# Optimization experiments

Hardware: AMD Instinct MI355X
Metric: run time of the kernel (lower is better)

The kernel has to match this reference:

```python
import jax, jax.numpy as jnp
import numpy as np

N_NODES = 50000


def gcn_conv(h, src, dst, W, b, n):
    # PyG GCNConv: x' = D^{-1/2} (A + I) D^{-1/2} (h W) + b
    x = h @ W  # [N, out]
    deg = jax.ops.segment_sum(jnp.ones_like(src, dtype=x.dtype), dst, num_segments=n) + 1.0  # self-loop
    dis = deg ** -0.5
    norm = dis[src] * dis[dst]  # [E]
    msg = x[src] * norm[:, None]  # [E, out]
    agg = jax.ops.segment_sum(msg, dst, num_segments=n)
    agg = agg + x * (dis * dis)[:, None]  # self-loop term: 1/deg_i * x_i
    return agg + b


def setup_inputs() -> dict:
    key = jax.random.key(0)
    ks = jax.random.split(key, 8)
    n, e = N_NODES, 800000
    d_in, d_rni, h = 128, 32, 256
    x = jax.random.normal(ks[0], (n, d_in), dtype=jnp.float32)
    rni = jax.random.normal(ks[1], (n, d_rni), dtype=jnp.float32)
    edge_index = jax.random.randint(ks[2], (2, e), 0, n, dtype=jnp.int64)
    s1 = (d_in + d_rni) ** -0.5
    s2 = h ** -0.5
    W1 = jax.random.normal(ks[3], (d_in + d_rni, h), dtype=jnp.float32) * s1
    b1 = jnp.zeros((h,), dtype=jnp.float32)
    W2 = jax.random.normal(ks[4], (h, h), dtype=jnp.float32) * s2
    b2 = jnp.zeros((h,), dtype=jnp.float32)
    W_out = jax.random.normal(ks[5], (h, h), dtype=jnp.float32) * s2
    b_out = jnp.zeros((h,), dtype=jnp.float32)
    return {"x": x, "rni": rni, "edge_index": edge_index, "W1": W1, "b1": b1,
            "W2": W2, "b2": b2, "W_out": W_out, "b_out": b_out}


def reference(x, rni, edge_index, W1, b1, W2, b2, W_out, b_out):
    n = x.shape[0]
    src, dst = edge_index[0], edge_index[1]
    h = jnp.concatenate([x, rni], axis=-1)  # RNI concat
    h = jax.nn.relu(gcn_conv(h, src, dst, W1, b1, n))
    h = jax.nn.relu(gcn_conv(h, src, dst, W2, b2, n))
    return h @ W_out + b_out
```

## Files before the change

kernel.cpp:

```cpp
#include <hip/hip_runtime.h>
#include <hip/hip_bf16.h>
#include <hip/hip_fp16.h>
#include <math.h>

#define D_IN   128
#define D_RNI  32
#define HID    256

typedef _Float16 half8 __attribute__((ext_vector_type(8)));
typedef float    f32x4 __attribute__((ext_vector_type(4)));

__global__ void k_prep(const unsigned int* __restrict__ ew, int nwords, int* __restrict__ mode,
                       const float* __restrict__ W1, __half* __restrict__ W1t,
                       const float* __restrict__ W2, __half* __restrict__ W2t,
                       const float* __restrict__ Wo, __half* __restrict__ Wot) {
    int b = blockIdx.x;
    if (b == 0) {
        __shared__ unsigned int red[256];
        unsigned int acc = 0;
        for (int i = threadIdx.x; i < 1024; i += 256) {
            int idx = 2 * i + 1;
            if (idx < nwords) acc |= ew[idx];
        }
        red[threadIdx.x] = acc;
        __syncthreads();
        for (int s = 128; s > 0; s >>= 1) {
            if (threadIdx.x < s) red[threadIdx.x] |= red[threadIdx.x + s];
            __syncthreads();
        }
        if (threadIdx.x == 0) *mode = (red[0] == 0u) ? 1 : 0;
        return;
    }
    int i = (b - 1) * 256 + threadIdx.x;
    const int T1 = (D_IN + D_RNI) * HID;
    const int T2 = HID * HID;
    if (i < T1) {
        int k = i / HID, nn = i - k * HID;
        W1t[(size_t)nn * (D_IN + D_RNI) + k] = __float2half(W1[i]);
    } else if (i < T1 + T2) {
        int j = i - T1;
        int k = j / HID, nn = j - k * HID;
        W2t[(size_t)nn * HID + k] = __float2half(W2[j]);
    } else {
        int j = i - T1 - T2;
        int k = j / HID, nn = j - k * HID;
        Wot[(size_t)nn * HID + k] = __float2half(Wo[j]);
    }
}

__global__ void k_count(const unsigned int* __restrict__ ew, const int* __restrict__ mode_p,
                        int* __restrict__ counts, int e) {
    int mode = *mode_p;
    int i = blockIdx.x * 256 + threadIdx.x;
    if (i >= e) return;
    int d = mode ? (int)ew[2 * ((size_t)e + i)] : (int)ew[(size_t)e + i];
    atomicAdd(&counts[d], 1);
}

__global__ __launch_bounds__(1024) void k_scan1(const int* __restrict__ counts,
                                                int* __restrict__ incl,
                                                int* __restrict__ bsum, int n) {
    __shared__ int sd[1024];
    int t = threadIdx.x;
    int i = blockIdx.x * 1024 + t;
    int v = (i < n) ? counts[i] : 0;
    sd[t] = v;
    __syncthreads();
    for (int off = 1; off < 1024; off <<= 1) {
        int tmp = (t >= off) ? sd[t - off] : 0;
        __syncthreads();
        sd[t] += tmp;
        __syncthreads();
    }
    if (i < n) incl[i] = sd[t];
    if (t == 1023) bsum[blockIdx.x] = sd[1023];
}

__global__ void k_scan3(const int* __restrict__ counts, const int* __restrict__ incl,
                        const int* __restrict__ bsum,
                        int* __restrict__ rowptr, int* __restrict__ cursor,
                        float* __restrict__ dis, int n, int nb) {
    __shared__ int pre_s, tot_s;
    int t = threadIdx.x;
    int c = (blockIdx.x * 256) >> 10;
    if (t < 64) {
        int v   = (t < nb) ? bsum[t] : 0;
        int pre = (t < c)  ? v : 0;
        int tot = v;
        #pragma unroll
        for (int m = 32; m > 0; m >>= 1) {
            pre += __shfl_down(pre, m);
            tot += __shfl_down(tot, m);
        }
        if (t == 0) { pre_s = pre; tot_s = tot; }
    }
    __syncthreads();
    int i = blockIdx.x * 256 + t;
    if (i >= n) return;
    int excl = incl[i] - counts[i] + pre_s;
    rowptr[i] = excl;
    cursor[i] = excl;
    dis[i] = 1.0f / sqrtf((float)(counts[i] + 1));
    if (i == 0) rowptr[n] = tot_s;
}

__global__ void k_scatter(const unsigned int* __restrict__ ew, const int* __restrict__ mode_p,
                          int* __restrict__ cursor, int* __restrict__ csr, int e) {
    int mode = *mode_p;
    int i = blockIdx.x * 256 + threadIdx.x;
    if (i >= e) return;
    int s, d;
    if (mode) {
        s = (int)ew[2 * (size_t)i];
        d = (int)ew[2 * ((size_t)e + i)];
    } else {
        s = (int)ew[(size_t)i];
        d = (int)ew[(size_t)e + i];
    }
    int pos = atomicAdd(&cursor[d], 1);
    csr[pos] = s;
}

#define KT 32
#define LSTR 40
template <bool A_F32, bool ADD_BIAS, bool HALF_OUT>
__global__ __launch_bounds__(512, 4) void k_mgemm(const void* __restrict__ Av, int strideA, int KA,
                                                  const void* __restrict__ A2v, int strideA2,
                                                  const __half* __restrict__ Bt,
                                                  const float* __restrict__ bias,
                                                  void* Cv, int M, int K) {
    __shared__ __half As[2][128 * LSTR];
    __shared__ __half Bs[2][256 * LSTR];
    int tid = threadIdx.x;
    int wave = tid >> 6, lane = tid & 63;
    int wm = wave >> 2, wn = wave & 3;
    int q = lane >> 4, m16 = lane & 15;
    int r0 = blockIdx.x * 128;

    int ar  = tid >> 2, akq = (tid & 3) * 8;
    int br  = tid >> 1, bkq = (tid & 1) * 16;

    int arow = r0 + ar; if (arow >= M) arow = M - 1;

    f32x4 acc[4][4] = {};

    float4 afr0, afr1;
    uint4  areg;
    uint4  breg0, breg1;

    auto loadA = [&](int k0) {
        if (A_F32) {
            const float* src; int stride, kk0;
            if (k0 < KA) { src = (const float*)Av;  stride = strideA;  kk0 = k0; }
            else         { src = (const float*)A2v; stride = strideA2; kk0 = k0 - KA; }
            const float* p = &src[(size_t)arow * stride + kk0 + akq];
            afr0 = *reinterpret_cast<const float4*>(p);
            afr1 = *reinterpret_cast<const float4*>(p + 4);
        } else {
            const __half* src = (const __half*)Av;
            areg = *reinterpret_cast<const uint4*>(&src[(size_t)arow * strideA + k0 + akq]);
        }
    };
    auto loadB = [&](int k0) {
        const __half* p = &Bt[(size_t)br * K + k0 + bkq];
        breg0 = *reinterpret_cast<const uint4*>(p);
        breg1 = *reinterpret_cast<const uint4*>(p + 8);
    };
    auto writeLDS = [&](int buf) {
        if (A_F32) {
            union { __half2 h2[4]; uint4 u; } uu;
            uu.h2[0] = __floats2half2_rn(afr0.x, afr0.y);
            uu.h2[1] = __floats2half2_rn(afr0.z, afr0.w);
            uu.h2[2] = __floats2half2_rn(afr1.x, afr1.y);
            uu.h2[3] = __floats2half2_rn(afr1.z, afr1.w);
            *reinterpret_cast<uint4*>(&As[buf][ar * LSTR + akq]) = uu.u;
        } else {
            *reinterpret_cast<uint4*>(&As[buf][ar * LSTR + akq]) = areg;
        }
        *reinterpret_cast<uint4*>(&Bs[buf][br * LSTR + bkq])     = breg0;
        *reinterpret_cast<uint4*>(&Bs[buf][br * LSTR + bkq + 8]) = breg1;
    };

    const int S = K / KT;
    loadA(0); loadB(0);
    writeLDS(0);
    __syncthreads();

    for (int t = 0; t < S; ++t) {
        int cur = t & 1;
        if (t + 1 < S) { loadA((t + 1) * KT); loadB((t + 1) * KT); }

        half8 af[4], bf[4];
        #pragma unroll
        for (int mi = 0; mi < 4; ++mi)
            af[mi] = *reinterpret_cast<const half8*>(&As[cur][(wm * 64 + mi * 16 + m16) * LSTR + q * 8]);
        #pragma unroll
        for (int ni = 0; ni < 4; ++ni)
            bf[ni] = *reinterpret_cast<const half8*>(&Bs[cur][(wn * 64 + ni * 16 + m16) * LSTR + q * 8]);
        #pragma unroll
        for (int mi = 0; mi < 4; ++mi)
            #pragma unroll
            for (int ni = 0; ni < 4; ++ni)
                acc[mi][ni] = __builtin_amdgcn_mfma_f32_16x16x32_f16(af[mi], bf[ni], acc[mi][ni], 0, 0, 0);

        if (t + 1 < S) writeLDS(cur ^ 1);
        __syncthreads();
    }

    #pragma unroll
    for (int mi = 0; mi < 4; ++mi) {
        #pragma unroll
        for (int r = 0; r < 4; ++r) {
            int row = r0 + wm * 64 + mi * 16 + q * 4 + r;
            if (row >= M) continue;
            #pragma unroll
            for (int ni = 0; ni < 4; ++ni) {
                int col = wn * 64 + ni * 16 + m16;
                float v = acc[mi][ni][r];
                if (ADD_BIAS) v += bias[col];
                if (HALF_OUT) ((__half*)Cv)[(size_t)row * HID + col] = __float2half(v);
                else          ((float*)Cv)[(size_t)row * HID + col] = v;
            }
        }
    }
}

__global__ __launch_bounds__(256) void k_agg(const __half* __restrict__ xh,
                                             const int* __restrict__ rowptr,
                                             const int* __restrict__ csr,
                                             const float* __restrict__ dis,
                                             const float* __restrict__ bias,
                                             __half* __restrict__ outh, int n) {
    int i = blockIdx.x * 4 + (threadIdx.x >> 6);
    if (i >= n) return;
    int lane = threadIdx.x & 63;
    int c4 = lane * 4;
    float disd = dis[i];
    int e0 = rowptr[i], e1 = rowptr[i + 1];

    float acc0, acc1, acc2, acc3;
    {
        uint2 v = *reinterpret_cast<const uint2*>(&xh[(size_t)i * HID + c4]);
        float2 f0 = __half22float2(*reinterpret_cast<__half2*>(&v.x));
        float2 f1 = __half22float2(*reinterpret_cast<__half2*>(&v.y));
        float ws = disd * disd;
        acc0 = f0.x * ws; acc1 = f0.y * ws; acc2 = f1.x * ws; acc3 = f1.y * ws;
    }

    for (int e = e0; e < e1; e += 64) {
        int cnt = min(64, e1 - e);
        int sreg = 0; float wreg = 0.0f;
        if (lane < cnt) {
            sreg = csr[e + lane];
            wreg = dis[sreg] * disd;
        }
        int j = 0;
        for (; j + 4 <= cnt; j += 4) {
            int   s0 = __shfl(sreg, j + 0), s1 = __shfl(sreg, j + 1);
            int   s2 = __shfl(sreg, j + 2), s3 = __shfl(sreg, j + 3);
            float w0 = __shfl(wreg, j + 0), w1 = __shfl(wreg, j + 1);
            float w2 = __shfl(wreg, j + 2), w3 = __shfl(wreg, j + 3);
            uint2 v0 = *reinterpret_cast<const uint2*>(&xh[(size_t)s0 * HID + c4]);
            uint2 v1 = *reinterpret_cast<const uint2*>(&xh[(size_t)s1 * HID + c4]);
            uint2 v2 = *reinterpret_cast<const uint2*>(&xh[(size_t)s2 * HID + c4]);
            uint2 v3 = *reinterpret_cast<const uint2*>(&xh[(size_t)s3 * HID + c4]);
            float2 a0 = __half22float2(*reinterpret_cast<__half2*>(&v0.x));
            float2 b0 = __half22float2(*reinterpret_cast<__half2*>(&v0.y));
            float2 a1 = __half22float2(*reinterpret_cast<__half2*>(&v1.x));
            float2 b1 = __half22float2(*reinterpret_cast<__half2*>(&v1.y));
            float2 a2 = __half22float2(*reinterpret_cast<__half2*>(&v2.x));
            float2 b2 = __half22float2(*reinterpret_cast<__half2*>(&v2.y));
            float2 a3 = __half22float2(*reinterpret_cast<__half2*>(&v3.x));
            float2 b3 = __half22float2(*reinterpret_cast<__half2*>(&v3.y));
            acc0 = fmaf(a0.x, w0, acc0); acc1 = fmaf(a0.y, w0, acc1);
            acc2 = fmaf(b0.x, w0, acc2); acc3 = fmaf(b0.y, w0, acc3);
            acc0 = fmaf(a1.x, w1, acc0); acc1 = fmaf(a1.y, w1, acc1);
            acc2 = fmaf(b1.x, w1, acc2); acc3 = fmaf(b1.y, w1, acc3);
            acc0 = fmaf(a2.x, w2, acc0); acc1 = fmaf(a2.y, w2, acc1);
            acc2 = fmaf(b2.x, w2, acc2); acc3 = fmaf(b2.y, w2, acc3);
            acc0 = fmaf(a3.x, w3, acc0); acc1 = fmaf(a3.y, w3, acc1);
            acc2 = fmaf(b3.x, w3, acc2); acc3 = fmaf(b3.y, w3, acc3);
        }
        for (; j < cnt; ++j) {
            int   s = __shfl(sreg, j);
            float w = __shfl(wreg, j);
            uint2 v = *reinterpret_cast<const uint2*>(&xh[(size_t)s * HID + c4]);
            float2 a = __half22float2(*reinterpret_cast<__half2*>(&v.x));
            float2 b = __half22float2(*reinterpret_cast<__half2*>(&v.y));
            acc0 = fmaf(a.x, w, acc0); acc1 = fmaf(a.y, w, acc1);
            acc2 = fmaf(b.x, w, acc2); acc3 = fmaf(b.y, w, acc3);
        }
    }

    float4 bb = *reinterpret_cast<const float4*>(&bias[c4]);
    union { __half2 h2[2]; uint2 u; } o;
    o.h2[0] = __floats2half2_rn(fmaxf(acc0 + bb.x, 0.0f), fmaxf(acc1 + bb.y, 0.0f));
    o.h2[1] = __floats2half2_rn(fmaxf(acc2 + bb.z, 0.0f), fmaxf(acc3 + bb.w, 0.0f));
    *reinterpret_cast<uint2*>(&outh[(size_t)i * HID + c4]) = o.u;
}

extern "C" void kernel_launch(void* const* d_in, const int* in_sizes, int n_in,
                              void* d_out, int out_size, void* d_ws, size_t ws_size,
                              hipStream_t stream) {
    const float* x     = (const float*)d_in[0];
    const float* rni   = (const float*)d_in[1];
    const unsigned int* ew = (const unsigned int*)d_in[2];
    const float* W1    = (const float*)d_in[3];
    const float* b1    = (const float*)d_in[4];
    const float* W2    = (const float*)d_in[5];
    const float* b2    = (const float*)d_in[6];
    const float* W_out = (const float*)d_in[7];
    const float* b_out = (const float*)d_in[8];
    float* out = (float*)d_out;

    const int n  = in_sizes[0] / D_IN;
    const int e  = in_sizes[2] / 2;
    const int nb = (n + 1023) / 1024;
    const int K1 = D_IN + D_RNI;

    char* ws = (char*)d_ws;
    size_t off = 0;
    auto carve = [&](size_t bytes) {
        char* p = ws + off;
        off = (off + bytes + 255) & ~(size_t)255;
        return p;
    };
    __half* xh    = (__half*)carve((size_t)n * HID * sizeof(__half));
    __half* h     = (__half*)carve((size_t)n * HID * sizeof(__half));
    __half* W1t   = (__half*)carve((size_t)K1 * HID * sizeof(__half));
    __half* W2t   = (__half*)carve((size_t)HID * HID * sizeof(__half));
    __half* Wot   = (__half*)carve((size_t)HID * HID * sizeof(__half));
    int*   counts = (int*)carve((size_t)n * sizeof(int));
    int*   incl   = (int*)carve((size_t)n * sizeof(int));
    int*   bsum   = (int*)carve((size_t)(nb + 1) * sizeof(int));
    int*   rowptr = (int*)carve((size_t)(n + 1) * sizeof(int));
    int*   cursor = (int*)carve((size_t)n * sizeof(int));
    float* dis    = (float*)carve((size_t)n * sizeof(float));
    int*   csr    = (int*)carve((size_t)e * sizeof(int));
    int*   mode   = (int*)carve(sizeof(int));
    (void)ws_size;

    const int eb = (e + 255) / 256;
    const int gemm_blocks = (n + 127) / 128;
    const int agg_blocks  = (n + 3) / 4;
    const int prep_blocks = 1 + (K1 * HID + 2 * HID * HID + 255) / 256;

    k_prep<<<prep_blocks, 256, 0, stream>>>(ew, 2 * e, mode, W1, W1t, W2, W2t, W_out, Wot);
    hipMemsetAsync(counts, 0, (size_t)n * sizeof(int), stream);
    k_count<<<eb, 256, 0, stream>>>(ew, mode, counts, e);
    k_scan1<<<nb, 1024, 0, stream>>>(counts, incl, bsum, n);
    k_scan3<<<(n + 255) / 256, 256, 0, stream>>>(counts, incl, bsum, rowptr, cursor, dis, n, nb);
    k_scatter<<<eb, 256, 0, stream>>>(ew, mode, cursor, csr, e);

    k_mgemm<true, false, true><<<gemm_blocks, 512, 0, stream>>>(x, D_IN, D_IN, rni, D_RNI,
                                                                W1t, nullptr, xh, n, K1);
    k_agg<<<agg_blocks, 256, 0, stream>>>(xh, rowptr, csr, dis, b1, h, n);

    k_mgemm<false, false, true><<<gemm_blocks, 512, 0, stream>>>(h, HID, HID, nullptr, 0,
                                                                 W2t, nullptr, xh, n, HID);
    k_agg<<<agg_blocks, 256, 0, stream>>>(xh, rowptr, csr, dis, b2, h, n);

    k_mgemm<false, true, false><<<gemm_blocks, 512, 0, stream>>>(h, HID, HID, nullptr, 0,
                                                                 Wot, b_out, out, n, HID);
}
```

Measured before the change: 361.4 us.

## Fuse CSR scatter with first GEMM launch and fold counts memset into prep

Merges the edge scatter kernel and the layer-1 GEMM into one launch, with block ranges split between GEMM tiles and scatter work. The memory-bound atomic scatter can then overlap with the compute-bound GEMM, and one launch is removed. The memset of the counts array moves into the weight-prep kernel, dropping another API call. Scatter blocks now reserve the GEMM's shared memory and launch bounds, which may limit how many scatter blocks are resident at once.

New measurement: 360.6 us. About the same (-0.2%).

```diff
diff --git a/kernel.cpp b/kernel.cpp
--- a/kernel.cpp
+++ b/kernel.cpp
@@ -13,7 +13,8 @@
 __global__ void k_prep(const unsigned int* __restrict__ ew, int nwords, int* __restrict__ mode,
                        const float* __restrict__ W1, __half* __restrict__ W1t,
                        const float* __restrict__ W2, __half* __restrict__ W2t,
-                       const float* __restrict__ Wo, __half* __restrict__ Wot) {
+                       const float* __restrict__ Wo, __half* __restrict__ Wot,
+                       int* __restrict__ counts, int n) {
     int b = blockIdx.x;
     if (b == 0) {
         __shared__ unsigned int red[256];
@@ -31,9 +32,10 @@
         if (threadIdx.x == 0) *mode = (red[0] == 0u) ? 1 : 0;
         return;
     }
-    int i = (b - 1) * 256 + threadIdx.x;
     const int T1 = (D_IN + D_RNI) * HID;
     const int T2 = HID * HID;
+    const int TW = T1 + 2 * T2;
+    int i = (b - 1) * 256 + threadIdx.x;
     if (i < T1) {
         int k = i / HID, nn = i - k * HID;
         W1t[(size_t)nn * (D_IN + D_RNI) + k] = __float2half(W1[i]);
@@ -41,10 +43,13 @@
         int j = i - T1;
         int k = j / HID, nn = j - k * HID;
         W2t[(size_t)nn * HID + k] = __float2half(W2[j]);
-    } else {
+    } else if (i < TW) {
         int j = i - T1 - T2;
         int k = j / HID, nn = j - k * HID;
         Wot[(size_t)nn * HID + k] = __float2half(Wo[j]);
+    } else {
+        int j = i - TW;
+        if (j < n) counts[j] = 0;
     }
 }
 
@@ -104,38 +109,22 @@
     if (i == 0) rowptr[n] = tot_s;
 }
 
-__global__ void k_scatter(const unsigned int* __restrict__ ew, const int* __restrict__ mode_p,
-                          int* __restrict__ cursor, int* __restrict__ csr, int e) {
-    int mode = *mode_p;
-    int i = blockIdx.x * 256 + threadIdx.x;
-    if (i >= e) return;
-    int s, d;
-    if (mode) {
-        s = (int)ew[2 * (size_t)i];
-        d = (int)ew[2 * ((size_t)e + i)];
-    } else {
-        s = (int)ew[(size_t)i];
-        d = (int)ew[(size_t)e + i];
-    }
-    int pos = atomicAdd(&cursor[d], 1);
-    csr[pos] = s;
-}
-
 #define KT 32
 #define LSTR 40
 template <bool A_F32, bool ADD_BIAS, bool HALF_OUT>
-__global__ __launch_bounds__(512, 4) void k_mgemm(const void* __restrict__ Av, int strideA, int KA,
-                                                  const void* __restrict__ A2v, int strideA2,
-                                                  const __half* __restrict__ Bt,
-                                                  const float* __restrict__ bias,
-                                                  void* Cv, int M, int K) {
+__device__ __forceinline__ void gemm_body(int blk,
+                                          const void* __restrict__ Av, int strideA, int KA,
+                                          const void* __restrict__ A2v, int strideA2,
+                                          const __half* __restrict__ Bt,
+                                          const float* __restrict__ bias,
+                                          void* Cv, int M, int K) {
     __shared__ __half As[2][128 * LSTR];
     __shared__ __half Bs[2][256 * LSTR];
     int tid = threadIdx.x;
     int wave = tid >> 6, lane = tid & 63;
     int wm = wave >> 2, wn = wave & 3;
     int q = lane >> 4, m16 = lane & 15;
-    int r0 = blockIdx.x * 128;
+    int r0 = blk * 128;
 
     int ar  = tid >> 2, akq = (tid & 3) * 8;
     int br  = tid >> 1, bkq = (tid & 1) * 16;
@@ -223,6 +212,41 @@
             }
         }
     }
+}
+
+template <bool A_F32, bool ADD_BIAS, bool HALF_OUT>
+__global__ __launch_bounds__(512, 4) void k_mgemm(const void* __restrict__ Av, int strideA, int KA,
+                                                  const void* __restrict__ A2v, int strideA2,
+                                                  const __half* __restrict__ Bt,
+                                                  const float* __restrict__ bias,
+                                                  void* Cv, int M, int K) {
+    gemm_body<A_F32, ADD_BIAS, HALF_OUT>(blockIdx.x, Av, strideA, KA, A2v, strideA2,
+                                         Bt, bias, Cv, M, K);
+}
+
+__global__ __launch_bounds__(512, 4) void k_scatgemm(
+        const unsigned int* __restrict__ ew, const int* __restrict__ mode_p,
+        int* __restrict__ cursor, int* __restrict__ csr, int e, int gemm_blocks,
+        const float* __restrict__ x, const float* __restrict__ rni,
+        const __half* __restrict__ W1t, __half* __restrict__ xh, int M, int K) {
+    if ((int)blockIdx.x < gemm_blocks) {
+        gemm_body<true, false, true>(blockIdx.x, x, D_IN, D_IN, rni, D_RNI,
+                                     W1t, nullptr, xh, M, K);
+        return;
+    }
+    int i = ((int)blockIdx.x - gemm_blocks) * 512 + (int)threadIdx.x;
+    if (i >= e) return;
+    int mode = *mode_p;
+    int s, d;
+    if (mode) {
+        s = (int)ew[2 * (size_t)i];
+        d = (int)ew[2 * ((size_t)e + i)];
+    } else {
+        s = (int)ew[(size_t)i];
+        d = (int)ew[(size_t)e + i];
+    }
+    int pos = atomicAdd(&cursor[d], 1);
+    csr[pos] = s;
 }
 
 __global__ __launch_bounds__(256) void k_agg(const __half* __restrict__ xh,
@@ -343,17 +367,20 @@
     const int eb = (e + 255) / 256;
     const int gemm_blocks = (n + 127) / 128;
     const int agg_blocks  = (n + 3) / 4;
-    const int prep_blocks = 1 + (K1 * HID + 2 * HID * HID + 255) / 256;
-
-    k_prep<<<prep_blocks, 256, 0, stream>>>(ew, 2 * e, mode, W1, W1t, W2, W2t, W_out, Wot);
-    hipMemsetAsync(counts, 0, (size_t)n * sizeof(int), stream);
+    const int TW = K1 * HID + 2 * HID * HID;
+    const int prep_blocks = 1 + (TW + n + 255) / 256;
+
+    k_prep<<<prep_blocks, 256, 0, stream>>>(ew, 2 * e, mode, W1, W1t, W2, W2t, W_out, Wot,
+                                            counts, n);
     k_count<<<eb, 256, 0, stream>>>(ew, mode, counts, e);
     k_scan1<<<nb, 1024, 0, stream>>>(counts, incl, bsum, n);
     k_scan3<<<(n + 255) / 256, 256, 0, stream>>>(counts, incl, bsum, rowptr, cursor, dis, n, nb);
-    k_scatter<<<eb, 256, 0, stream>>>(ew, mode, cursor, csr, e);
-
-    k_mgemm<true, false, true><<<gemm_blocks, 512, 0, stream>>>(x, D_IN, D_IN, rni, D_RNI,
-                                                                W1t, nullptr, xh, n, K1);
+
+    {
+        const int sb = (e + 511) / 512;
+        k_scatgemm<<<gemm_blocks + sb, 512, 0, stream>>>(ew, mode, cursor, csr, e, gemm_blocks,
+                                                         x, rni, W1t, xh, n, K1);
+    }
     k_agg<<<agg_blocks, 256, 0, stream>>>(xh, rowptr, csr, dis, b1, h, n);
 
     k_mgemm<false, false, true><<<gemm_blocks, 512, 0, stream>>>(h, HID, HID, nullptr, 0,
```
